# Optimization experiments

Measured on AMD Instinct MI355X. Metric: run time of the kernel, lower is better.

## Reference

```python
import math
import jax, jax.numpy as jnp
import numpy as np

C_CURV = 0.5  # Poincare ball curvature c (StablePoincareBall default)


def expmap0(u, c=C_CURV):
    """StablePoincareBall.expmap0: tangent at origin -> ball, with norm clamps."""
    sqrt_c = math.sqrt(c)
    u_norm = jnp.clip(jnp.linalg.norm(u, axis=-1, keepdims=True), 1e-8, 5.0)
    res = jnp.tanh(sqrt_c * u_norm) / sqrt_c * (u / u_norm)
    max_allowed = 0.95 / sqrt_c
    rn = jnp.linalg.norm(res, axis=-1, keepdims=True)
    scale = jnp.where(rn > max_allowed, max_allowed / rn, jnp.ones_like(rn))
    return res * scale


def poincare_pairwise_dist(x, p, c=C_CURV):
    """Geodesic dist d(x_i, p_j) = (2/sqrt(c)) atanh(sqrt(c) ||(-x) (+) p||).
    Uses the closed form for ||mobius_add(-x, p)||^2 in terms of ||x||^2, ||p||^2,
    <x,p> so only [B,C] intermediates are formed (no [B,C,D] broadcast).
    """
    x2 = jnp.sum(x * x, axis=-1, keepdims=True)        # [B,1]
    p2 = jnp.sum(p * p, axis=-1)[None, :]              # [1,C]
    mdot = -(x @ p.T)                                  # <-x, p>  [B,C]
    A = 1.0 + 2.0 * c * mdot + c * p2                  # coeff of (-x)
    Bc = 1.0 - c * x2                                  # coeff of p
    den = 1.0 + 2.0 * c * mdot + (c * c) * x2 * p2
    num2 = A * A * x2 + 2.0 * A * Bc * mdot + Bc * Bc * p2
    m2 = jnp.maximum(num2, 0.0) / jnp.maximum(den * den, 1e-15)
    sqrt_c = math.sqrt(c)
    arg = jnp.clip(sqrt_c * jnp.sqrt(m2 + 1e-15), 0.0, 1.0 - 1e-5)
    return (2.0 / sqrt_c) * jnp.arctanh(arg)


def setup_inputs() -> dict:
    key = jax.random.key(0)
    k1, k2 = jax.random.split(key)
    B, C, D = 128, 4096, 1024
    # inputs live on the Poincare ball: map random tangents via expmap0
    x = expmap0(0.5 * jax.random.normal(k1, (B, D), dtype=jnp.float32))
    # prototypes per __init__: expmap0(randn*0.1) then rescale norm to 1/sqrt(c)-1e-5
    init_tangent = 0.1 * jax.random.normal(k2, (C, D), dtype=jnp.float32)
    protos = expmap0(init_tangent)
    max_norm = 1.0 / math.sqrt(C_CURV) - 1e-5
    nrm = jnp.clip(jnp.linalg.norm(protos, axis=-1, keepdims=True), 1e-8)
    protos = protos * (max_norm / nrm)
    return {"x": x, "prototypes": protos}


def reference(x, prototypes):
    # logits = -geodesic distance to each class prototype, [B, num_classes]
    return -poincare_pairwise_dist(x, prototypes)
```

## Files before the change

kernel.cpp:

```cpp
#include <hip/hip_runtime.h>
#include <hip/hip_bf16.h>
#include <math.h>


#define DDIM 1024
#define CDIM 4096

using f32x4  = __attribute__((ext_vector_type(4))) float;
using bf16x8 = __attribute__((ext_vector_type(8))) short;

__device__ inline ushort toBfU(float f) {
  __hip_bfloat16 h = __float2bfloat16(f);
  return *reinterpret_cast<ushort*>(&h);
}

__global__ __launch_bounds__(256, 2) void hyper_k32b(
    const float* __restrict__ x, const float* __restrict__ p,
    float* __restrict__ out) {
  __shared__ __align__(16) char xs[2][8192];
  __shared__ __align__(16) char ps[2][8192];
  __shared__ float x2s[32], p2s[32];

  const int tid  = threadIdx.x;
  const int lane = tid & 63;
  const int w    = __builtin_amdgcn_readfirstlane(tid >> 6);
  const int r15  = lane & 15, g = lane >> 4;

  const int bid  = blockIdx.x;
  const int swz  = ((bid & 7) << 6) | (bid >> 3);
  const int rg   = swz & 3, cg = swz >> 2;
  const int rbase = rg * 32, cbase = cg * 32;

  const int srow = tid >> 3;
  const float* gx = x + (size_t)(rbase + srow) * DDIM + ((tid & 7) << 4);
  const float* gp = p + (size_t)(cbase + srow) * DDIM + ((tid & 7) << 4);
  const int ssw = (srow & 7) << 4;
  const int sb0 = srow * 256 + ((((tid & 7) << 5) +  0) ^ ssw);
  const int sb1 = srow * 256 + ((((tid & 7) << 5) + 16) ^ ssw);

  float sx = 0.f, sp = 0.f;
  f32x4 acc00 = {0.f,0.f,0.f,0.f}, acc01 = acc00, acc10 = acc00, acc11 = acc00;
  f32x4 xa[4], pa[4];

#define LOADS(c)                                                              \
  { _Pragma("unroll")                                                         \
    for (int i = 0; i < 4; ++i) {                                             \
      xa[i] = *(const f32x4*)(gx + (c) * 128 + i * 4);                        \
      pa[i] = *(const f32x4*)(gp + (c) * 128 + i * 4);                        \
    } }

#define SSQ4(v) (fmaf((v)[3],(v)[3],fmaf((v)[2],(v)[2],fmaf((v)[1],(v)[1],(v)[0]*(v)[0]))))

#define PACKW(a, b, dst)                                                      \
  { bf16x8 _t;                                                                \
    _t[0]=(short)toBfU((a)[0]); _t[1]=(short)toBfU((a)[1]);                   \
    _t[2]=(short)toBfU((a)[2]); _t[3]=(short)toBfU((a)[3]);                   \
    _t[4]=(short)toBfU((b)[0]); _t[5]=(short)toBfU((b)[1]);                   \
    _t[6]=(short)toBfU((b)[2]); _t[7]=(short)toBfU((b)[3]);                   \
    *(bf16x8*)(dst) = _t; }

#define WRITES(BUF)                                                           \
  { sx += SSQ4(xa[0]) + SSQ4(xa[1]) + SSQ4(xa[2]) + SSQ4(xa[3]);              \
    sp += SSQ4(pa[0]) + SSQ4(pa[1]) + SSQ4(pa[2]) + SSQ4(pa[3]);              \
    PACKW(xa[0], xa[1], &xs[BUF][sb0])                                        \
    PACKW(xa[2], xa[3], &xs[BUF][sb1])                                        \
    PACKW(pa[0], pa[1], &ps[BUF][sb0])                                        \
    PACKW(pa[2], pa[3], &ps[BUF][sb1])                                        \
  }

#define COMPUTE(BUF)                                                          \
  { const int ba = ((w << 6) + (g << 4)) ^ ((r15 & 7) << 4);                  \
    const bf16x8 A0  = *(const bf16x8*)&xs[BUF][r15 * 256 + ba];              \
    const bf16x8 A1  = *(const bf16x8*)&xs[BUF][(16 + r15) * 256 + ba];       \
    const bf16x8 Bq0 = *(const bf16x8*)&ps[BUF][r15 * 256 + ba];              \
    const bf16x8 Bq1 = *(const bf16x8*)&ps[BUF][(16 + r15) * 256 + ba];       \
    acc00 = __builtin_amdgcn_mfma_f32_16x16x32_bf16(A0, Bq0, acc00, 0, 0, 0); \
    acc10 = __builtin_amdgcn_mfma_f32_16x16x32_bf16(A1, Bq0, acc10, 0, 0, 0); \
    acc01 = __builtin_amdgcn_mfma_f32_16x16x32_bf16(A0, Bq1, acc01, 0, 0, 0); \
    acc11 = __builtin_amdgcn_mfma_f32_16x16x32_bf16(A1, Bq1, acc11, 0, 0, 0); \
  }

  LOADS(0)
  WRITES(0)
  __syncthreads();

  #pragma unroll
  for (int c = 0; c < 8; ++c) {
    if (c < 7) LOADS(c + 1)
    COMPUTE(c & 1)
    if (c < 7) WRITES((c + 1) & 1)
    __syncthreads();
  }

  sx += __shfl_xor(sx, 1, 64); sx += __shfl_xor(sx, 2, 64); sx += __shfl_xor(sx, 4, 64);
  sp += __shfl_xor(sp, 1, 64); sp += __shfl_xor(sp, 2, 64); sp += __shfl_xor(sp, 4, 64);
  if ((lane & 7) == 0) { x2s[srow] = sx; p2s[srow] = sp; }

  f32x4* cb = (f32x4*)xs;
  cb[(w * 4 + 0) * 64 + lane] = acc00;
  cb[(w * 4 + 1) * 64 + lane] = acc10;
  cb[(w * 4 + 2) * 64 + lane] = acc01;
  cb[(w * 4 + 3) * 64 + lane] = acc11;
  __syncthreads();

  f32x4 fa = cb[(0 * 4 + w) * 64 + lane];
  fa += cb[(1 * 4 + w) * 64 + lane];
  fa += cb[(2 * 4 + w) * 64 + lane];
  fa += cb[(3 * 4 + w) * 64 + lane];

  const int qr = w & 1, qc = w >> 1;
  const float p2 = p2s[qc * 16 + r15];
  #pragma unroll
  for (int i = 0; i < 4; ++i) {
    const int  rloc = qr * 16 + g * 4 + i;
    const float dot = fa[i];
    const float x2  = x2s[rloc];
    const float A   = 1.0f - dot + 0.5f  * p2;
    const float Bc  = 1.0f - 0.5f * x2;
    const float den = 1.0f - dot + 0.25f * x2 * p2;
    float num2 = A * A * x2 - 2.0f * A * Bc * dot + Bc * Bc * p2;
    float m2   = fmaxf(num2, 0.0f) / fmaxf(den * den, 1e-15f);
    float arg  = fminf(0.7071067811865476f * sqrtf(m2 + 1e-15f), 0.99999f);
    out[(size_t)(rbase + rloc) * CDIM + cbase + qc * 16 + r15] =
        -1.4142135623730951f * __logf((1.0f + arg) / (1.0f - arg));
  }
}

extern "C" void kernel_launch(void* const* d_in, const int* in_sizes, int n_in,
                              void* d_out, int out_size, void* d_ws, size_t ws_size,
                              hipStream_t stream) {
  const float* x = (const float*)d_in[0];
  const float* p = (const float*)d_in[1];
  float* out = (float*)d_out;
  hyper_k32b<<<dim3(512), dim3(256), 0, stream>>>(x, p, out);
}
```

Baseline: 14.78 us.

## Retile to 64x16 blocks with whole prototype tile hoisted into LDS

Changes the block tile from 32x32 to 64 rows by 16 prototypes. The full 16x1024 prototype slab is loaded and converted to bf16 once up front into a 32KB LDS buffer, while x tiles stay double-buffered per K chunk. Each wave now owns a 16x16 output tile and accumulates across the full K instead of splitting K across waves, which removes the cross-wave LDS reduction of partial accumulators. The cost is a larger LDS footprint of about 64KB per block, which may reduce occupancy, a serialized upfront prototype load, and more x traffic per output.

```diff
diff --git a/kernel.cpp b/kernel.cpp
--- a/kernel.cpp
+++ b/kernel.cpp
@@ -14,12 +14,12 @@
   return *reinterpret_cast<ushort*>(&h);
 }
 
-__global__ __launch_bounds__(256, 2) void hyper_k32b(
+__global__ __launch_bounds__(256, 2) void hyper_phoist(
     const float* __restrict__ x, const float* __restrict__ p,
     float* __restrict__ out) {
-  __shared__ __align__(16) char xs[2][8192];
-  __shared__ __align__(16) char ps[2][8192];
-  __shared__ float x2s[32], p2s[32];
+  __shared__ __align__(16) char xs[2][16384];
+  __shared__ __align__(16) char ps[32768];
+  __shared__ float x2s[64], p2s[16];
 
   const int tid  = threadIdx.x;
   const int lane = tid & 63;
@@ -28,25 +28,28 @@
 
   const int bid  = blockIdx.x;
   const int swz  = ((bid & 7) << 6) | (bid >> 3);
-  const int rg   = swz & 3, cg = swz >> 2;
-  const int rbase = rg * 32, cbase = cg * 32;
+  const int cg = swz >> 1, rg = swz & 1;
+  const int rbase = rg * 64, cbase = cg * 16;
 
-  const int srow = tid >> 3;
-  const float* gx = x + (size_t)(rbase + srow) * DDIM + ((tid & 7) << 4);
-  const float* gp = p + (size_t)(cbase + srow) * DDIM + ((tid & 7) << 4);
-  const int ssw = (srow & 7) << 4;
-  const int sb0 = srow * 256 + ((((tid & 7) << 5) +  0) ^ ssw);
-  const int sb1 = srow * 256 + ((((tid & 7) << 5) + 16) ^ ssw);
+  const int tr  = tid >> 4;
+  const int t16 = tid & 15;
+  const float* gx = x + (size_t)(rbase + tr) * DDIM + t16 * 8;
+  const float* gp = p + (size_t)(cbase + tr) * DDIM;
+  const int xwz = (t16 << 4);
+  const int pswz = (tr & 7) << 4;
 
-  float sx = 0.f, sp = 0.f;
-  f32x4 acc00 = {0.f,0.f,0.f,0.f}, acc01 = acc00, acc10 = acc00, acc11 = acc00;
-  f32x4 xa[4], pa[4];
+  float sx0 = 0.f, sx1 = 0.f, sx2 = 0.f, sx3 = 0.f, sp = 0.f;
+  f32x4 acc = {0.f, 0.f, 0.f, 0.f};
+  f32x4 xa[4][2];
 
-#define LOADS(c)                                                              \
+  const int arow = (w << 4) + r15;
+  const int swr  = (r15 & 7) << 4;
+
+#define LOADS_X(c)                                                            \
   { _Pragma("unroll")                                                         \
     for (int i = 0; i < 4; ++i) {                                             \
-      xa[i] = *(const f32x4*)(gx + (c) * 128 + i * 4);                        \
-      pa[i] = *(const f32x4*)(gp + (c) * 128 + i * 4);                        \
+      xa[i][0] = *(const f32x4*)(gx + (size_t)i * 16 * DDIM + (c) * 128);     \
+      xa[i][1] = *(const f32x4*)(gx + (size_t)i * 16 * DDIM + (c) * 128 + 4); \
     } }
 
 #define SSQ4(v) (fmaf((v)[3],(v)[3],fmaf((v)[2],(v)[2],fmaf((v)[1],(v)[1],(v)[0]*(v)[0]))))
@@ -59,61 +62,74 @@
     _t[6]=(short)toBfU((b)[2]); _t[7]=(short)toBfU((b)[3]);                   \
     *(bf16x8*)(dst) = _t; }
 
-#define WRITES(BUF)                                                           \
-  { sx += SSQ4(xa[0]) + SSQ4(xa[1]) + SSQ4(xa[2]) + SSQ4(xa[3]);              \
-    sp += SSQ4(pa[0]) + SSQ4(pa[1]) + SSQ4(pa[2]) + SSQ4(pa[3]);              \
-    PACKW(xa[0], xa[1], &xs[BUF][sb0])                                        \
-    PACKW(xa[2], xa[3], &xs[BUF][sb1])                                        \
-    PACKW(pa[0], pa[1], &ps[BUF][sb0])                                        \
-    PACKW(pa[2], pa[3], &ps[BUF][sb1])                                        \
+#define WRITES_X(BUF)                                                         \
+  { sx0 += SSQ4(xa[0][0]) + SSQ4(xa[0][1]);                                   \
+    sx1 += SSQ4(xa[1][0]) + SSQ4(xa[1][1]);                                   \
+    sx2 += SSQ4(xa[2][0]) + SSQ4(xa[2][1]);                                   \
+    sx3 += SSQ4(xa[3][0]) + SSQ4(xa[3][1]);                                   \
+    _Pragma("unroll")                                                         \
+    for (int i = 0; i < 4; ++i) {                                             \
+      const int row = i * 16 + tr;                                            \
+      PACKW(xa[i][0], xa[i][1], &xs[BUF][row * 256 + (xwz ^ ((row & 7) << 4))]) \
+    } }
+
+#define COMPUTE(BUF, c)                                                       \
+  { _Pragma("unroll")                                                         \
+    for (int ks = 0; ks < 4; ++ks) {                                          \
+      const int ao = (ks * 64 + g * 16) ^ swr;                                \
+      const bf16x8 a = *(const bf16x8*)&xs[BUF][arow * 256 + ao];             \
+      const bf16x8 b = *(const bf16x8*)&ps[r15 * 2048 + (((c) * 256 + ks * 64 + g * 16) ^ swr)]; \
+      acc = __builtin_amdgcn_mfma_f32_16x16x32_bf16(a, b, acc, 0, 0, 0);      \
+    } }
+
+  {
+    f32x4 pa[8][2];
+    #pragma unroll
+    for (int i = 0; i < 8; ++i) {
+      pa[i][0] = *(const f32x4*)(gp + (t16 + 16 * i) * 8);
+      pa[i][1] = *(const f32x4*)(gp + (t16 + 16 * i) * 8 + 4);
+    }
+    LOADS_X(0)
+    #pragma unroll
+    for (int i = 0; i < 8; ++i) {
+      sp += SSQ4(pa[i][0]) + SSQ4(pa[i][1]);
+      const int s = t16 + 16 * i;
+      PACKW(pa[i][0], pa[i][1], &ps[tr * 2048 + ((s << 4) ^ pswz)])
+    }
+    WRITES_X(0)
   }
-
-#define COMPUTE(BUF)                                                          \
-  { const int ba = ((w << 6) + (g << 4)) ^ ((r15 & 7) << 4);                  \
-    const bf16x8 A0  = *(const bf16x8*)&xs[BUF][r15 * 256 + ba];              \
-    const bf16x8 A1  = *(const bf16x8*)&xs[BUF][(16 + r15) * 256 + ba];       \
-    const bf16x8 Bq0 = *(const bf16x8*)&ps[BUF][r15 * 256 + ba];              \
-    const bf16x8 Bq1 = *(const bf16x8*)&ps[BUF][(16 + r15) * 256 + ba];       \
-    acc00 = __builtin_amdgcn_mfma_f32_16x16x32_bf16(A0, Bq0, acc00, 0, 0, 0); \
-    acc10 = __builtin_amdgcn_mfma_f32_16x16x32_bf16(A1, Bq0, acc10, 0, 0, 0); \
-    acc01 = __builtin_amdgcn_mfma_f32_16x16x32_bf16(A0, Bq1, acc01, 0, 0, 0); \
-    acc11 = __builtin_amdgcn_mfma_f32_16x16x32_bf16(A1, Bq1, acc11, 0, 0, 0); \
-  }
-
-  LOADS(0)
-  WRITES(0)
   __syncthreads();
 
   #pragma unroll
   for (int c = 0; c < 8; ++c) {
-    if (c < 7) LOADS(c + 1)
-    COMPUTE(c & 1)
-    if (c < 7) WRITES((c + 1) & 1)
+    if (c < 7) LOADS_X(c + 1)
+    COMPUTE(c & 1, c)
+    if (c < 7) WRITES_X((c + 1) & 1)
     __syncthreads();
   }
 
-  sx += __shfl_xor(sx, 1, 64); sx += __shfl_xor(sx, 2, 64); sx += __shfl_xor(sx, 4, 64);
-  sp += __shfl_xor(sp, 1, 64); sp += __shfl_xor(sp, 2, 64); sp += __shfl_xor(sp, 4, 64);
-  if ((lane & 7) == 0) { x2s[srow] = sx; p2s[srow] = sp; }
-
-  f32x4* cb = (f32x4*)xs;
-  cb[(w * 4 + 0) * 64 + lane] = acc00;
-  cb[(w * 4 + 1) * 64 + lane] = acc10;
-  cb[(w * 4 + 2) * 64 + lane] = acc01;
-  cb[(w * 4 + 3) * 64 + lane] = acc11;
+  #pragma unroll
+  for (int off = 8; off > 0; off >>= 1) {
+    sx0 += __shfl_xor(sx0, off, 64);
+    sx1 += __shfl_xor(sx1, off, 64);
+    sx2 += __shfl_xor(sx2, off, 64);
+    sx3 += __shfl_xor(sx3, off, 64);
+    sp  += __shfl_xor(sp,  off, 64);
+  }
+  if ((lane & 15) == 0) {
+    x2s[ 0 + tr] = sx0;
+    x2s[16 + tr] = sx1;
+    x2s[32 + tr] = sx2;
+    x2s[48 + tr] = sx3;
+    p2s[tr] = sp;
+  }
   __syncthreads();
 
-  f32x4 fa = cb[(0 * 4 + w) * 64 + lane];
-  fa += cb[(1 * 4 + w) * 64 + lane];
-  fa += cb[(2 * 4 + w) * 64 + lane];
-  fa += cb[(3 * 4 + w) * 64 + lane];
-
-  const int qr = w & 1, qc = w >> 1;
-  const float p2 = p2s[qc * 16 + r15];
+  const float p2 = p2s[r15];
   #pragma unroll
   for (int i = 0; i < 4; ++i) {
-    const int  rloc = qr * 16 + g * 4 + i;
-    const float dot = fa[i];
+    const int  rloc = (w << 4) + (g << 2) + i;
+    const float dot = acc[i];
     const float x2  = x2s[rloc];
     const float A   = 1.0f - dot + 0.5f  * p2;
     const float Bc  = 1.0f - 0.5f * x2;
@@ -121,7 +137,7 @@
     float num2 = A * A * x2 - 2.0f * A * Bc * dot + Bc * Bc * p2;
     float m2   = fmaxf(num2, 0.0f) / fmaxf(den * den, 1e-15f);
     float arg  = fminf(0.7071067811865476f * sqrtf(m2 + 1e-15f), 0.99999f);
-    out[(size_t)(rbase + rloc) * CDIM + cbase + qc * 16 + r15] =
+    out[(size_t)(rbase + rloc) * CDIM + cbase + r15] =
         -1.4142135623730951f * __logf((1.0f + arg) / (1.0f - arg));
   }
 }
@@ -132,5 +148,5 @@
   const float* x = (const float*)d_in[0];
   const float* p = (const float*)d_in[1];
   float* out = (float*)d_out;
-  hyper_k32b<<<dim3(512), dim3(256), 0, stream>>>(x, p, out);
+  hyper_phoist<<<dim3(512), dim3(256), 0, stream>>>(x, p, out);
 }
```

Measured after the change: 14.88 us. No clear change (+0.7%).

## Quantize operands to FP8 and stage full K tile in LDS

Applied to the files above, without the earlier changes.

Operands are now converted to fp8 instead of bf16. The whole 32x1024 tiles of x and prototypes are written once into a padded LDS buffer, followed by a single barrier. Each wave then computes its own 16x16 output quadrant over the full K with fp8 MFMAs, which removes the per-chunk double-buffer syncs and the cross-wave accumulator reduction. This trades the load/compute overlap and much of the dot-product precision for simpler scheduling. fp8 rounding error may push results near the ball boundary outside tolerance.

```diff
diff --git a/kernel.cpp b/kernel.cpp
--- a/kernel.cpp
+++ b/kernel.cpp
@@ -1,25 +1,20 @@
 #include <hip/hip_runtime.h>
-#include <hip/hip_bf16.h>
 #include <math.h>
 
 
 #define DDIM 1024
 #define CDIM 4096
+#define RSTR 1040
+#define PSOFF 33280
 
-using f32x4  = __attribute__((ext_vector_type(4))) float;
-using bf16x8 = __attribute__((ext_vector_type(8))) short;
+using f32x4 = __attribute__((ext_vector_type(4))) float;
+using i32x4 = __attribute__((ext_vector_type(4))) int;
 
-__device__ inline ushort toBfU(float f) {
-  __hip_bfloat16 h = __float2bfloat16(f);
-  return *reinterpret_cast<ushort*>(&h);
-}
-
-__global__ __launch_bounds__(256, 2) void hyper_k32b(
-    const float* __restrict__ x, const float* __restrict__ p,
-    float* __restrict__ out) {
-  __shared__ __align__(16) char xs[2][8192];
-  __shared__ __align__(16) char ps[2][8192];
-  __shared__ float x2s[32], p2s[32];
+__global__ __launch_bounds__(256, 2) void hyper_fp8(
+    const float* __restrict__ x, const float* __restrict__ p, float* __restrict__ out) {
+  __shared__ __align__(16) char smem[66816];
+  float* x2s = (float*)(smem + 66560);
+  float* p2s = (float*)(smem + 66560 + 128);
 
   const int tid  = threadIdx.x;
   const int lane = tid & 63;
@@ -32,88 +27,61 @@
   const int rbase = rg * 32, cbase = cg * 32;
 
   const int srow = tid >> 3;
-  const float* gx = x + (size_t)(rbase + srow) * DDIM + ((tid & 7) << 4);
-  const float* gp = p + (size_t)(cbase + srow) * DDIM + ((tid & 7) << 4);
-  const int ssw = (srow & 7) << 4;
-  const int sb0 = srow * 256 + ((((tid & 7) << 5) +  0) ^ ssw);
-  const int sb1 = srow * 256 + ((((tid & 7) << 5) + 16) ^ ssw);
+  const int l8   = tid & 7;
+  const float* gx = x + (size_t)(rbase + srow) * DDIM + l8 * 16;
+  const float* gp = p + (size_t)(cbase + srow) * DDIM + l8 * 16;
+  char* xd = smem + srow * RSTR + l8 * 16;
+  char* pd = smem + PSOFF + srow * RSTR + l8 * 16;
 
   float sx = 0.f, sp = 0.f;
-  f32x4 acc00 = {0.f,0.f,0.f,0.f}, acc01 = acc00, acc10 = acc00, acc11 = acc00;
-  f32x4 xa[4], pa[4];
-
-#define LOADS(c)                                                              \
-  { _Pragma("unroll")                                                         \
-    for (int i = 0; i < 4; ++i) {                                             \
-      xa[i] = *(const f32x4*)(gx + (c) * 128 + i * 4);                        \
-      pa[i] = *(const f32x4*)(gp + (c) * 128 + i * 4);                        \
-    } }
-
-#define SSQ4(v) (fmaf((v)[3],(v)[3],fmaf((v)[2],(v)[2],fmaf((v)[1],(v)[1],(v)[0]*(v)[0]))))
-
-#define PACKW(a, b, dst)                                                      \
-  { bf16x8 _t;                                                                \
-    _t[0]=(short)toBfU((a)[0]); _t[1]=(short)toBfU((a)[1]);                   \
-    _t[2]=(short)toBfU((a)[2]); _t[3]=(short)toBfU((a)[3]);                   \
-    _t[4]=(short)toBfU((b)[0]); _t[5]=(short)toBfU((b)[1]);                   \
-    _t[6]=(short)toBfU((b)[2]); _t[7]=(short)toBfU((b)[3]);                   \
-    *(bf16x8*)(dst) = _t; }
-
-#define WRITES(BUF)                                                           \
-  { sx += SSQ4(xa[0]) + SSQ4(xa[1]) + SSQ4(xa[2]) + SSQ4(xa[3]);              \
-    sp += SSQ4(pa[0]) + SSQ4(pa[1]) + SSQ4(pa[2]) + SSQ4(pa[3]);              \
-    PACKW(xa[0], xa[1], &xs[BUF][sb0])                                        \
-    PACKW(xa[2], xa[3], &xs[BUF][sb1])                                        \
-    PACKW(pa[0], pa[1], &ps[BUF][sb0])                                        \
-    PACKW(pa[2], pa[3], &ps[BUF][sb1])                                        \
-  }
-
-#define COMPUTE(BUF)                                                          \
-  { const int ba = ((w << 6) + (g << 4)) ^ ((r15 & 7) << 4);                  \
-    const bf16x8 A0  = *(const bf16x8*)&xs[BUF][r15 * 256 + ba];              \
-    const bf16x8 A1  = *(const bf16x8*)&xs[BUF][(16 + r15) * 256 + ba];       \
-    const bf16x8 Bq0 = *(const bf16x8*)&ps[BUF][r15 * 256 + ba];              \
-    const bf16x8 Bq1 = *(const bf16x8*)&ps[BUF][(16 + r15) * 256 + ba];       \
-    acc00 = __builtin_amdgcn_mfma_f32_16x16x32_bf16(A0, Bq0, acc00, 0, 0, 0); \
-    acc10 = __builtin_amdgcn_mfma_f32_16x16x32_bf16(A1, Bq0, acc10, 0, 0, 0); \
-    acc01 = __builtin_amdgcn_mfma_f32_16x16x32_bf16(A0, Bq1, acc01, 0, 0, 0); \
-    acc11 = __builtin_amdgcn_mfma_f32_16x16x32_bf16(A1, Bq1, acc11, 0, 0, 0); \
-  }
-
-  LOADS(0)
-  WRITES(0)
-  __syncthreads();
 
   #pragma unroll
-  for (int c = 0; c < 8; ++c) {
-    if (c < 7) LOADS(c + 1)
-    COMPUTE(c & 1)
-    if (c < 7) WRITES((c + 1) & 1)
-    __syncthreads();
+  for (int m = 0; m < 8; ++m) {
+    f32x4 xv[4], pv[4];
+    #pragma unroll
+    for (int j = 0; j < 4; ++j) {
+      xv[j] = *(const f32x4*)(gx + m * 128 + j * 4);
+      pv[j] = *(const f32x4*)(gp + m * 128 + j * 4);
+    }
+    i32x4 xq, pq;
+    #pragma unroll
+    for (int j = 0; j < 4; ++j) {
+      sx = fmaf(xv[j][0], xv[j][0], sx); sx = fmaf(xv[j][1], xv[j][1], sx);
+      sx = fmaf(xv[j][2], xv[j][2], sx); sx = fmaf(xv[j][3], xv[j][3], sx);
+      sp = fmaf(pv[j][0], pv[j][0], sp); sp = fmaf(pv[j][1], pv[j][1], sp);
+      sp = fmaf(pv[j][2], pv[j][2], sp); sp = fmaf(pv[j][3], pv[j][3], sp);
+      int xw = __builtin_amdgcn_cvt_pk_fp8_f32(xv[j][0], xv[j][1], 0, false);
+      xw     = __builtin_amdgcn_cvt_pk_fp8_f32(xv[j][2], xv[j][3], xw, true);
+      int pw = __builtin_amdgcn_cvt_pk_fp8_f32(pv[j][0], pv[j][1], 0, false);
+      pw     = __builtin_amdgcn_cvt_pk_fp8_f32(pv[j][2], pv[j][3], pw, true);
+      xq[j] = xw; pq[j] = pw;
+    }
+    *(i32x4*)(xd + m * 128) = xq;
+    *(i32x4*)(pd + m * 128) = pq;
   }
 
   sx += __shfl_xor(sx, 1, 64); sx += __shfl_xor(sx, 2, 64); sx += __shfl_xor(sx, 4, 64);
   sp += __shfl_xor(sp, 1, 64); sp += __shfl_xor(sp, 2, 64); sp += __shfl_xor(sp, 4, 64);
   if ((lane & 7) == 0) { x2s[srow] = sx; p2s[srow] = sp; }
 
-  f32x4* cb = (f32x4*)xs;
-  cb[(w * 4 + 0) * 64 + lane] = acc00;
-  cb[(w * 4 + 1) * 64 + lane] = acc10;
-  cb[(w * 4 + 2) * 64 + lane] = acc01;
-  cb[(w * 4 + 3) * 64 + lane] = acc11;
   __syncthreads();
 
-  f32x4 fa = cb[(0 * 4 + w) * 64 + lane];
-  fa += cb[(1 * 4 + w) * 64 + lane];
-  fa += cb[(2 * 4 + w) * 64 + lane];
-  fa += cb[(3 * 4 + w) * 64 + lane];
+  const int qr = w & 1, qc = w >> 1;
+  const char* abase = smem + (qr * 16 + r15) * RSTR + g * 8;
+  const char* bbase = smem + PSOFF + (qc * 16 + r15) * RSTR + g * 8;
+  f32x4 acc = {0.f, 0.f, 0.f, 0.f};
+  #pragma unroll
+  for (int kk = 0; kk < 32; ++kk) {
+    const long a = *(const long*)(abase + kk * 32);
+    const long b = *(const long*)(bbase + kk * 32);
+    acc = __builtin_amdgcn_mfma_f32_16x16x32_fp8_fp8(a, b, acc, 0, 0, 0);
+  }
 
-  const int qr = w & 1, qc = w >> 1;
   const float p2 = p2s[qc * 16 + r15];
   #pragma unroll
   for (int i = 0; i < 4; ++i) {
-    const int  rloc = qr * 16 + g * 4 + i;
-    const float dot = fa[i];
+    const int  rloc = qr * 16 + (g << 2) + i;
+    const float dot = acc[i];
     const float x2  = x2s[rloc];
     const float A   = 1.0f - dot + 0.5f  * p2;
     const float Bc  = 1.0f - 0.5f * x2;
@@ -132,5 +100,5 @@
   const float* x = (const float*)d_in[0];
   const float* p = (const float*)d_in[1];
   float* out = (float*)d_out;
-  hyper_k32b<<<dim3(512), dim3(256), 0, stream>>>(x, p, out);
+  hyper_fp8<<<dim3(512), dim3(256), 0, stream>>>(x, p, out);
 }
```

After: 16.01 us. 1.08x slower.
